# Kernel optimization log

Measured on AMD Instinct MI355X. Metric: run time of the kernel, lower is better.

## Reference

```python
import jax, jax.numpy as jnp
import numpy as np

NUM_LATENTS = 1
NUM_EMBEDDINGS = 2048
EMBEDDING_DIM = 64
DECAY = 0.99
EPS = 1e-5


def setup_inputs() -> dict:
    key = jax.random.key(0)
    k1, k2 = jax.random.split(key)
    x = jax.random.normal(k1, (65536, NUM_LATENTS * EMBEDDING_DIM), dtype=jnp.float32)
    embedding = jax.random.normal(k2, (NUM_LATENTS, NUM_EMBEDDINGS, EMBEDDING_DIM), dtype=jnp.float32)
    cluster_size = jnp.ones((NUM_LATENTS, NUM_EMBEDDINGS), dtype=jnp.float32)
    return {"input": x, "embedding": embedding, "cluster_size": cluster_size}


def reference(input, embedding, cluster_size):
    L, K, D = embedding.shape
    flat = input.reshape(-1, L, D)  # (N, L, D)
    # Squared euclidean distances (N, L, K), expanded form of (x - e)^2 sum over D
    x_sq = jnp.sum(flat * flat, axis=-1, keepdims=True)           # (N, L, 1)
    e_sq = jnp.sum(embedding * embedding, axis=-1)[None]          # (1, L, K)
    cross = jnp.einsum('nld,lkd->nlk', flat, embedding)           # (N, L, K)
    distances = x_sq - 2.0 * cross + e_sq
    encoding_indices = jnp.argmin(distances, axis=-1)             # (N, L)
    # decode: gather codebook vectors
    quantized = embedding[jnp.arange(L)[None, :], encoding_indices]  # (N, L, D)
    encodings = jax.nn.one_hot(encoding_indices, K, dtype=input.dtype)  # (N, L, K)
    # --- EMA update (training branch, non-simple, laplace smoothing) ---
    onehot_sum = jnp.sum(encodings, axis=0)                       # (L, K)
    dw = jnp.einsum('nlk,nld->lkd', encodings, flat)              # (L, K, D)
    new_cluster_size = DECAY * cluster_size + (1.0 - DECAY) * onehot_sum
    n = jnp.sum(new_cluster_size, axis=-1, keepdims=True)
    cs = (new_cluster_size + EPS) / (n + K * EPS) * n
    new_embedding = DECAY * embedding + (1.0 - DECAY) * (dw / cs[..., None])
    # --- losses / outputs ---
    q = quantized.reshape(input.shape)
    commitment_loss = jnp.mean((q - input) ** 2)
    quantized_st = input + jax.lax.stop_gradient(q - input)
    avg_probs = jnp.mean(encodings, axis=0)                       # (L, K)
    perplexity = jnp.exp(-jnp.sum(avg_probs * jnp.log(avg_probs + 1e-10) / L))
    return (quantized_st, encodings, commitment_loss, perplexity, new_embedding, new_cluster_size)
```

## Files before the change

### kernel.cpp

```cpp
#include <hip/hip_runtime.h>
#include <math.h>

#define NROWS 65536
#define KEMB  2048
#define DIM   64
#define DECAYF 0.99f
#define OMDF   0.01f
#define EPSF   1e-5f

#define WS_DW    0
#define WS_CNT   131072
#define WS_LOSS  133120
#define WS_ESQ   133632
#define WS_SCALE 135680
#define WS_IDX   137728
#define WS_SORT  203264
#define WS_START 268800
#define WS_CUR   270852

#define OUT_Q    0
#define OUT_ENC  4194304
#define OUT_LOSS 138412032
#define OUT_PERP 138412033
#define OUT_NE   138412034
#define OUT_NCS  138543106

typedef float f32x4 __attribute__((ext_vector_type(4)));

__global__ __launch_bounds__(256) void k0_prep(const float* __restrict__ x,
                                               const float* __restrict__ E,
                                               float* __restrict__ ws,
                                               float* __restrict__ out) {
    int g = blockIdx.x * 256 + threadIdx.x;
    if (g == 0) ws[WS_LOSS] = 0.f;
    if (g < 32768) {
        float4 z = make_float4(0.f, 0.f, 0.f, 0.f);
        ((float4*)(ws + WS_DW))[g] = z;
    }
    if (g < KEMB) {
        ((unsigned int*)ws)[WS_CNT + g] = 0u;
        const float4* e4 = (const float4*)(E + (size_t)g * DIM);
        float s0 = 0.f, s1 = 0.f, s2 = 0.f, s3 = 0.f;
#pragma unroll
        for (int j = 0; j < 16; j++) {
            float4 v = e4[j];
            s0 = fmaf(v.x, v.x, s0); s1 = fmaf(v.y, v.y, s1);
            s2 = fmaf(v.z, v.z, s2); s3 = fmaf(v.w, v.w, s3);
        }
        ws[WS_ESQ + g] = (s0 + s1) + (s2 + s3);
    }
    {
        const float4* x4 = (const float4*)(x + (size_t)g * DIM);
        float s0 = 0.f, s1 = 0.f, s2 = 0.f, s3 = 0.f;
#pragma unroll
        for (int j = 0; j < 16; j++) {
            float4 v = x4[j];
            s0 = fmaf(v.x, v.x, s0); s1 = fmaf(v.y, v.y, s1);
            s2 = fmaf(v.z, v.z, s2); s3 = fmaf(v.w, v.w, s3);
        }
        out[OUT_NE + g] = (s0 + s1) + (s2 + s3);
    }
}

__global__ __launch_bounds__(256, 2) void k1_main(const float* __restrict__ x,
                                                  const float* __restrict__ E,
                                                  float* __restrict__ ws,
                                                  float* __restrict__ out) {
    __shared__ float sxT[64 * 128];
    __shared__ float seT[64 * 128];

    const int t = threadIdx.x;
    const int b = blockIdx.x;
    const int tx = t & 15;
    const int ty = t >> 4;

    float xsq[8];
    {
        const float2* xs2 = (const float2*)(out + OUT_NE + (size_t)b * 128 + ty * 8);
#pragma unroll
        for (int j = 0; j < 4; j++) {
            float2 v = xs2[j];
            xsq[2 * j] = v.x; xsq[2 * j + 1] = v.y;
        }
    }

    const int kl = t & 127;
    const int dchi = t >> 7;
    {
        const float4* x4 = (const float4*)x;
#pragma unroll
        for (int i = 0; i < 8; i++) {
            int dc = dchi + 2 * i;
            float4 v = x4[((size_t)b * 128 + kl) * 16 + dc];
            sxT[(4 * dc + 0) * 128 + kl] = v.x;
            sxT[(4 * dc + 1) * 128 + kl] = v.y;
            sxT[(4 * dc + 2) * 128 + kl] = v.z;
            sxT[(4 * dc + 3) * 128 + kl] = v.w;
        }
    }

    const int c = kl >> 2;
    const int fo = (((c & 1) << 4) + (c >> 1)) * 4 + (kl & 3);
    const float4* e4 = (const float4*)E;

    float4 pv[8];
#pragma unroll
    for (int i = 0; i < 8; i++)
        pv[i] = e4[((size_t)kl) * 16 + (dchi + 2 * i)];

    float best[8];
    int bidx[8];
#pragma unroll
    for (int rr = 0; rr < 8; rr++) { best[rr] = 3.4e38f; bidx[rr] = 0; }

    f32x4* __restrict__ encz = (f32x4*)(out + OUT_ENC);
    const int g = b * 256 + t;

    for (int pass = 0; pass < 16; pass++) {
        __syncthreads();
        {
#pragma unroll
            for (int i = 0; i < 8; i++) {
                int dc = dchi + 2 * i;
                seT[(4 * dc + 0) * 128 + fo] = pv[i].x;
                seT[(4 * dc + 1) * 128 + fo] = pv[i].y;
                seT[(4 * dc + 2) * 128 + fo] = pv[i].z;
                seT[(4 * dc + 3) * 128 + fo] = pv[i].w;
            }
        }
        __syncthreads();

        if (pass < 15) {
#pragma unroll
            for (int i = 0; i < 8; i++)
                pv[i] = e4[((size_t)(pass + 1) * 128 + kl) * 16 + (dchi + 2 * i)];
        }

        {
            f32x4 z = (f32x4)(0.f);
#pragma unroll
            for (int j = 0; j < 16; j++)
                __builtin_nontemporal_store(z, encz + (size_t)(pass * 16 + j) * 131072 + g);
        }

        float acc[8][8];
#pragma unroll
        for (int rr = 0; rr < 8; rr++)
#pragma unroll
            for (int cc = 0; cc < 8; cc++) acc[rr][cc] = 0.f;

        const float* xb  = sxT + ty * 8;
        const float* ebA = seT + tx * 4;
        const float* ebB = seT + 64 + tx * 4;
#pragma unroll 2
        for (int d = 0; d < 64; d++) {
            f32x4 a0 = *(const f32x4*)(xb + d * 128);
            f32x4 a1 = *(const f32x4*)(xb + d * 128 + 4);
            f32x4 b0 = *(const f32x4*)(ebA + d * 128);
            f32x4 b1 = *(const f32x4*)(ebB + d * 128);
#pragma unroll
            for (int rr = 0; rr < 4; rr++) {
#pragma unroll
                for (int cc = 0; cc < 4; cc++) {
                    acc[rr][cc]         = fmaf(a0[rr], b0[cc], acc[rr][cc]);
                    acc[rr][cc + 4]     = fmaf(a0[rr], b1[cc], acc[rr][cc + 4]);
                    acc[rr + 4][cc]     = fmaf(a1[rr], b0[cc], acc[rr + 4][cc]);
                    acc[rr + 4][cc + 4] = fmaf(a1[rr], b1[cc], acc[rr + 4][cc + 4]);
                }
            }
        }

        const float4* esq4 = (const float4*)(ws + WS_ESQ + pass * 128 + tx * 8);
        float4 eq0 = esq4[0], eq1 = esq4[1];
        float eq[8] = {eq0.x, eq0.y, eq0.z, eq0.w, eq1.x, eq1.y, eq1.z, eq1.w};
        const int kb = pass * 128 + tx * 8;
#pragma unroll
        for (int rr = 0; rr < 8; rr++)
#pragma unroll
            for (int cc = 0; cc < 8; cc++) {
                float dist = fmaf(-2.f, acc[rr][cc], xsq[rr]) + eq[cc];
                if (dist < best[rr]) { best[rr] = dist; bidx[rr] = kb + cc; }
            }
    }

    __syncthreads();
    int* sIdx = (int*)seT;
#pragma unroll
    for (int rr = 0; rr < 8; rr++) {
        float bd = best[rr]; int bi = bidx[rr];
#pragma unroll
        for (int m = 1; m < 16; m <<= 1) {
            float od = __shfl_xor(bd, m, 64);
            int   oi = __shfl_xor(bi, m, 64);
            if (od < bd || (od == bd && oi < bi)) { bd = od; bi = oi; }
        }
        if (tx == 0) sIdx[ty * 8 + rr] = bi;
    }
    __syncthreads();

    if (t < 128) {
        const int row = b * 128 + t;
        const int bi = sIdx[t];
        ((int*)ws)[WS_IDX + row] = bi;
        atomicAdd(((unsigned int*)ws) + WS_CNT + bi, 1u);
        const float4* ebb = (const float4*)(E + (size_t)bi * DIM);
        const float4* xr4 = (const float4*)(x + (size_t)row * DIM);
        float4* qo = (float4*)(out + OUT_Q + (size_t)row * DIM);
        float l0 = 0.f, l1 = 0.f, l2 = 0.f, l3 = 0.f;
#pragma unroll
        for (int j = 0; j < 16; j++) {
            float4 ev = ebb[j];
            float4 xv = xr4[j];
            qo[j] = ev;
            float d0 = ev.x - xv.x, d1 = ev.y - xv.y;
            float d2 = ev.z - xv.z, d3 = ev.w - xv.w;
            l0 = fmaf(d0, d0, l0); l1 = fmaf(d1, d1, l1);
            l2 = fmaf(d2, d2, l2); l3 = fmaf(d3, d3, l3);
        }
        float lsum = (l0 + l1) + (l2 + l3);
#pragma unroll
        for (int o = 32; o; o >>= 1) lsum += __shfl_down(lsum, o, 64);
        if ((t & 63) == 0) unsafeAtomicAdd(ws + WS_LOSS, lsum);
    }
}

__global__ __launch_bounds__(256) void k2bs(const float* __restrict__ cs_in,
                                            float* __restrict__ ws,
                                            float* __restrict__ out) {
    __shared__ unsigned int sscan[256];
    __shared__ float sred[8];
    __shared__ float s_n;
    const int t = threadIdx.x;
    const unsigned int* cnt = ((const unsigned int*)ws) + WS_CNT;

    unsigned int c[8];
    unsigned int tot = 0;
#pragma unroll
    for (int j = 0; j < 8; j++) { c[j] = cnt[t * 8 + j]; tot += c[j]; }
    sscan[t] = tot;
    __syncthreads();
    for (int off = 1; off < 256; off <<= 1) {
        unsigned int v = (t >= off) ? sscan[t - off] : 0u;
        __syncthreads();
        sscan[t] += v;
        __syncthreads();
    }
    unsigned int run = sscan[t] - tot;
    unsigned int* starts = ((unsigned int*)ws) + WS_START;
    unsigned int* cur = ((unsigned int*)ws) + WS_CUR;
#pragma unroll
    for (int j = 0; j < 8; j++) {
        starts[t * 8 + j] = run;
        cur[t * 8 + j] = run;
        run += c[j];
    }
    if (t == 255) starts[KEMB] = run;

    float* ncs_out = out + OUT_NCS;
    float ln = 0.f, lent = 0.f;
    float ncs_v[8];
#pragma unroll
    for (int j = 0; j < 8; j++) {
        int k = t * 8 + j;
        float cf = (float)c[j];
        float ncs = DECAYF * cs_in[k] + OMDF * cf;
        ncs_out[k] = ncs;
        ncs_v[j] = ncs;
        ln += ncs;
        float p = cf * (1.0f / 65536.0f);
        lent = fmaf(p, logf(p + 1e-10f), lent);
    }
#pragma unroll
    for (int o = 32; o; o >>= 1) {
        ln += __shfl_down(ln, o, 64);
        lent += __shfl_down(lent, o, 64);
    }
    if ((t & 63) == 0) { sred[t >> 6] = ln; sred[4 + (t >> 6)] = lent; }
    __syncthreads();
    if (t == 0) {
        float n = (sred[0] + sred[1]) + (sred[2] + sred[3]);
        float ent = (sred[4] + sred[5]) + (sred[6] + sred[7]);
        s_n = n;
        out[OUT_LOSS] = ws[WS_LOSS] * (1.0f / 4194304.0f);
        out[OUT_PERP] = expf(-ent);
    }
    __syncthreads();
    float n = s_n;
    float denom = n + (float)KEMB * EPSF;
#pragma unroll
    for (int j = 0; j < 8; j++) {
        int k = t * 8 + j;
        float cs = (ncs_v[j] + EPSF) / denom * n;
        ws[WS_SCALE + k] = OMDF / cs;
    }
}

__global__ __launch_bounds__(256) void k2c_scatter(const int* __restrict__ idxp,
                                                   float* __restrict__ ws,
                                                   float* __restrict__ out) {
    const int g = blockIdx.x * 256 + threadIdx.x;
    int4 v = ((const int4*)idxp)[g];
    unsigned int* cur = ((unsigned int*)ws) + WS_CUR;
    int* sorted = ((int*)ws) + WS_SORT;
    float* __restrict__ enc = out + OUT_ENC;
    const int row = 4 * g;
    unsigned int p0 = atomicAdd(&cur[v.x], 1u);
    unsigned int p1 = atomicAdd(&cur[v.y], 1u);
    unsigned int p2 = atomicAdd(&cur[v.z], 1u);
    unsigned int p3 = atomicAdd(&cur[v.w], 1u);
    sorted[p0] = row + 0;
    sorted[p1] = row + 1;
    sorted[p2] = row + 2;
    sorted[p3] = row + 3;
    enc[(size_t)(row + 0) * KEMB + v.x] = 1.0f;
    enc[(size_t)(row + 1) * KEMB + v.y] = 1.0f;
    enc[(size_t)(row + 2) * KEMB + v.z] = 1.0f;
    enc[(size_t)(row + 3) * KEMB + v.w] = 1.0f;
}

__global__ __launch_bounds__(256) void k2d_dw(const float* __restrict__ x,
                                              const int* __restrict__ idxp,
                                              float* __restrict__ ws) {
    const int t = threadIdx.x;
    const int lane = t & 63;
    const int w = blockIdx.x * 4 + (t >> 6);
    const int base = w * 64;
    const int* sorted = ((const int*)ws) + WS_SORT;

    int rid = sorted[base + lane];
    int code_l = idxp[rid];

    float acc = 0.f;
    int cur = __shfl(code_l, 0, 64);
#pragma unroll 8
    for (int i = 0; i < 64; i++) {
        int row = __shfl(rid, i, 64);
        int code = __shfl(code_l, i, 64);
        if (code != cur) {
            unsafeAtomicAdd(ws + WS_DW + (size_t)cur * DIM + lane, acc);
            acc = 0.f;
            cur = code;
        }
        acc += x[(size_t)row * DIM + lane];
    }
    unsafeAtomicAdd(ws + WS_DW + (size_t)cur * DIM + lane, acc);
}

__global__ __launch_bounds__(256) void k4_embed(const float* __restrict__ E,
                                                const float* __restrict__ ws,
                                                float* __restrict__ out) {
    int gq = blockIdx.x * 256 + threadIdx.x;
    const float4* E4 = (const float4*)E;
    const float4* dw4 = (const float4*)(ws + WS_DW);
    float2* o2 = (float2*)(out + OUT_NE);
    int k = gq >> 4;
    float sc = ws[WS_SCALE + k];
    float4 e = E4[gq];
    float4 d = dw4[gq];
    float2 r0, r1;
    r0.x = fmaf(d.x, sc, DECAYF * e.x);
    r0.y = fmaf(d.y, sc, DECAYF * e.y);
    r1.x = fmaf(d.z, sc, DECAYF * e.z);
    r1.y = fmaf(d.w, sc, DECAYF * e.w);
    o2[2 * gq + 0] = r0;
    o2[2 * gq + 1] = r1;
}

extern "C" void kernel_launch(void* const* d_in, const int* in_sizes, int n_in,
                              void* d_out, int out_size, void* d_ws, size_t ws_size,
                              hipStream_t stream) {
    const float* x = (const float*)d_in[0];
    const float* E = (const float*)d_in[1];
    const float* cs = (const float*)d_in[2];
    float* out = (float*)d_out;
    float* ws = (float*)d_ws;
    const int* idxp = ((const int*)ws) + WS_IDX;

    hipLaunchKernelGGL(k0_prep, dim3(256), dim3(256), 0, stream, x, E, ws, out);
    hipLaunchKernelGGL(k1_main, dim3(512), dim3(256), 0, stream, x, E, ws, out);
    hipLaunchKernelGGL(k2bs, dim3(1), dim3(256), 0, stream, cs, ws, out);
    hipLaunchKernelGGL(k2c_scatter, dim3(64), dim3(256), 0, stream, idxp, ws, out);
    hipLaunchKernelGGL(k2d_dw, dim3(256), dim3(256), 0, stream, x, idxp, ws);
    hipLaunchKernelGGL(k4_embed, dim3(128), dim3(256), 0, stream, E, ws, out);
}
```

Measured before the change: 294.4 us.

## Widen codebook tile to 256 codes and fuse row norms and one-hot writes

The distance kernel now processes 256 codebook entries per pass, using an 8x16 register tile per thread and two 32-wide depth halves staged through shared memory. This raises FMA work per shared-memory load and halves the number of passes. Row squared norms are now computed in k1_main while x is loaded into shared memory, so k0_prep no longer reads x. The one-hot 1.0 is written in k1_main right after that block zeroes its own encoding rows, which removes the scatter write from k2c_scatter. The cost is much higher register pressure from 128 accumulators per thread, which could cause spills or lower occupancy.

```diff
diff --git a/kernel.cpp b/kernel.cpp
--- a/kernel.cpp
+++ b/kernel.cpp
@@ -27,16 +27,11 @@
 
 typedef float f32x4 __attribute__((ext_vector_type(4)));
 
-__global__ __launch_bounds__(256) void k0_prep(const float* __restrict__ x,
-                                               const float* __restrict__ E,
-                                               float* __restrict__ ws,
-                                               float* __restrict__ out) {
+__global__ __launch_bounds__(256) void k0_prep(const float* __restrict__ E,
+                                               float* __restrict__ ws) {
     int g = blockIdx.x * 256 + threadIdx.x;
     if (g == 0) ws[WS_LOSS] = 0.f;
-    if (g < 32768) {
-        float4 z = make_float4(0.f, 0.f, 0.f, 0.f);
-        ((float4*)(ws + WS_DW))[g] = z;
-    }
+    ((float4*)(ws + WS_DW))[g] = make_float4(0.f, 0.f, 0.f, 0.f);
     if (g < KEMB) {
         ((unsigned int*)ws)[WS_CNT + g] = 0u;
         const float4* e4 = (const float4*)(E + (size_t)g * DIM);
@@ -48,17 +43,6 @@
             s2 = fmaf(v.z, v.z, s2); s3 = fmaf(v.w, v.w, s3);
         }
         ws[WS_ESQ + g] = (s0 + s1) + (s2 + s3);
-    }
-    {
-        const float4* x4 = (const float4*)(x + (size_t)g * DIM);
-        float s0 = 0.f, s1 = 0.f, s2 = 0.f, s3 = 0.f;
-#pragma unroll
-        for (int j = 0; j < 16; j++) {
-            float4 v = x4[j];
-            s0 = fmaf(v.x, v.x, s0); s1 = fmaf(v.y, v.y, s1);
-            s2 = fmaf(v.z, v.z, s2); s3 = fmaf(v.w, v.w, s3);
-        }
-        out[OUT_NE + g] = (s0 + s1) + (s2 + s3);
     }
 }
 
@@ -67,46 +51,47 @@
                                                   float* __restrict__ ws,
                                                   float* __restrict__ out) {
     __shared__ float sxT[64 * 128];
-    __shared__ float seT[64 * 128];
+    __shared__ float seT[32 * 256];
+    __shared__ float sxq[256];
 
     const int t = threadIdx.x;
     const int b = blockIdx.x;
     const int tx = t & 15;
     const int ty = t >> 4;
 
+    {
+        const int rl = t & 127;
+        const int dhi2 = t >> 7;
+        const float4* x4 = (const float4*)x;
+        float s0 = 0.f, s1 = 0.f, s2 = 0.f, s3 = 0.f;
+#pragma unroll
+        for (int i = 0; i < 8; i++) {
+            int dc = dhi2 + 2 * i;
+            float4 v = x4[((size_t)b * 128 + rl) * 16 + dc];
+            sxT[(4 * dc + 0) * 128 + rl] = v.x;
+            sxT[(4 * dc + 1) * 128 + rl] = v.y;
+            sxT[(4 * dc + 2) * 128 + rl] = v.z;
+            sxT[(4 * dc + 3) * 128 + rl] = v.w;
+            s0 = fmaf(v.x, v.x, s0); s1 = fmaf(v.y, v.y, s1);
+            s2 = fmaf(v.z, v.z, s2); s3 = fmaf(v.w, v.w, s3);
+        }
+        sxq[dhi2 * 128 + rl] = (s0 + s1) + (s2 + s3);
+    }
+
+    const int sbase = (((t >> 2) & 3) << 6) + ((t >> 4) << 2) + (t & 3);
+    const float4* e4 = (const float4*)E;
+
+    float4 pv[8];
+#pragma unroll
+    for (int j = 0; j < 8; j++)
+        pv[j] = e4[(size_t)t * 16 + j];
+
+    __syncthreads();
+
     float xsq[8];
-    {
-        const float2* xs2 = (const float2*)(out + OUT_NE + (size_t)b * 128 + ty * 8);
-#pragma unroll
-        for (int j = 0; j < 4; j++) {
-            float2 v = xs2[j];
-            xsq[2 * j] = v.x; xsq[2 * j + 1] = v.y;
-        }
-    }
-
-    const int kl = t & 127;
-    const int dchi = t >> 7;
-    {
-        const float4* x4 = (const float4*)x;
-#pragma unroll
-        for (int i = 0; i < 8; i++) {
-            int dc = dchi + 2 * i;
-            float4 v = x4[((size_t)b * 128 + kl) * 16 + dc];
-            sxT[(4 * dc + 0) * 128 + kl] = v.x;
-            sxT[(4 * dc + 1) * 128 + kl] = v.y;
-            sxT[(4 * dc + 2) * 128 + kl] = v.z;
-            sxT[(4 * dc + 3) * 128 + kl] = v.w;
-        }
-    }
-
-    const int c = kl >> 2;
-    const int fo = (((c & 1) << 4) + (c >> 1)) * 4 + (kl & 3);
-    const float4* e4 = (const float4*)E;
-
-    float4 pv[8];
-#pragma unroll
-    for (int i = 0; i < 8; i++)
-        pv[i] = e4[((size_t)kl) * 16 + (dchi + 2 * i)];
+#pragma unroll
+    for (int rr = 0; rr < 8; rr++)
+        xsq[rr] = sxq[ty * 8 + rr] + sxq[128 + ty * 8 + rr];
 
     float best[8];
     int bidx[8];
@@ -114,77 +99,84 @@
     for (int rr = 0; rr < 8; rr++) { best[rr] = 3.4e38f; bidx[rr] = 0; }
 
     f32x4* __restrict__ encz = (f32x4*)(out + OUT_ENC);
-    const int g = b * 256 + t;
-
-    for (int pass = 0; pass < 16; pass++) {
-        __syncthreads();
-        {
-#pragma unroll
-            for (int i = 0; i < 8; i++) {
-                int dc = dchi + 2 * i;
-                seT[(4 * dc + 0) * 128 + fo] = pv[i].x;
-                seT[(4 * dc + 1) * 128 + fo] = pv[i].y;
-                seT[(4 * dc + 2) * 128 + fo] = pv[i].z;
-                seT[(4 * dc + 3) * 128 + fo] = pv[i].w;
-            }
-        }
-        __syncthreads();
-
-        if (pass < 15) {
-#pragma unroll
-            for (int i = 0; i < 8; i++)
-                pv[i] = e4[((size_t)(pass + 1) * 128 + kl) * 16 + (dchi + 2 * i)];
-        }
-
-        {
-            f32x4 z = (f32x4)(0.f);
-#pragma unroll
-            for (int j = 0; j < 16; j++)
-                __builtin_nontemporal_store(z, encz + (size_t)(pass * 16 + j) * 131072 + g);
-        }
-
-        float acc[8][8];
+
+    for (int pass = 0; pass < 8; pass++) {
+        float acc[8][16];
 #pragma unroll
         for (int rr = 0; rr < 8; rr++)
 #pragma unroll
-            for (int cc = 0; cc < 8; cc++) acc[rr][cc] = 0.f;
-
-        const float* xb  = sxT + ty * 8;
-        const float* ebA = seT + tx * 4;
-        const float* ebB = seT + 64 + tx * 4;
-#pragma unroll 2
-        for (int d = 0; d < 64; d++) {
-            f32x4 a0 = *(const f32x4*)(xb + d * 128);
-            f32x4 a1 = *(const f32x4*)(xb + d * 128 + 4);
-            f32x4 b0 = *(const f32x4*)(ebA + d * 128);
-            f32x4 b1 = *(const f32x4*)(ebB + d * 128);
-#pragma unroll
-            for (int rr = 0; rr < 4; rr++) {
-#pragma unroll
-                for (int cc = 0; cc < 4; cc++) {
-                    acc[rr][cc]         = fmaf(a0[rr], b0[cc], acc[rr][cc]);
-                    acc[rr][cc + 4]     = fmaf(a0[rr], b1[cc], acc[rr][cc + 4]);
-                    acc[rr + 4][cc]     = fmaf(a1[rr], b0[cc], acc[rr + 4][cc]);
-                    acc[rr + 4][cc + 4] = fmaf(a1[rr], b1[cc], acc[rr + 4][cc + 4]);
+            for (int m = 0; m < 16; m++) acc[rr][m] = 0.f;
+
+        for (int dh = 0; dh < 2; dh++) {
+            if (pass + dh) __syncthreads();
+#pragma unroll
+            for (int j = 0; j < 8; j++) {
+                seT[(4 * j + 0) * 256 + sbase] = pv[j].x;
+                seT[(4 * j + 1) * 256 + sbase] = pv[j].y;
+                seT[(4 * j + 2) * 256 + sbase] = pv[j].z;
+                seT[(4 * j + 3) * 256 + sbase] = pv[j].w;
+            }
+            __syncthreads();
+
+            {
+                int h = pass * 2 + dh + 1;
+                if (h < 16) {
+#pragma unroll
+                    for (int j = 0; j < 8; j++)
+                        pv[j] = e4[((size_t)((h >> 1) * 256 + t)) * 16 + (h & 1) * 8 + j];
                 }
             }
-        }
-
-        const float4* esq4 = (const float4*)(ws + WS_ESQ + pass * 128 + tx * 8);
-        float4 eq0 = esq4[0], eq1 = esq4[1];
-        float eq[8] = {eq0.x, eq0.y, eq0.z, eq0.w, eq1.x, eq1.y, eq1.z, eq1.w};
-        const int kb = pass * 128 + tx * 8;
+
+            if (dh == 0) {
+                f32x4 z = (f32x4)(0.f);
+#pragma unroll
+                for (int j = 0; j < 32; j++)
+                    __builtin_nontemporal_store(z,
+                        encz + (size_t)b * 65536 + pass * 8192 + j * 256 + t);
+            }
+
+            const float* xbase = sxT + dh * 32 * 128 + ty * 8;
+            for (int dd = 0; dd < 32; dd++) {
+                const float* sb = seT + dd * 256;
+                f32x4 a0 = *(const f32x4*)(xbase + dd * 128);
+                f32x4 a1 = *(const f32x4*)(xbase + dd * 128 + 4);
+                f32x4 b0 = *(const f32x4*)(sb + tx * 4);
+                f32x4 b1 = *(const f32x4*)(sb + 64 + tx * 4);
+                f32x4 b2 = *(const f32x4*)(sb + 128 + tx * 4);
+                f32x4 b3 = *(const f32x4*)(sb + 192 + tx * 4);
+#pragma unroll
+                for (int rr = 0; rr < 4; rr++) {
+#pragma unroll
+                    for (int cc = 0; cc < 4; cc++) {
+                        acc[rr][cc]          = fmaf(a0[rr], b0[cc], acc[rr][cc]);
+                        acc[rr][4 + cc]      = fmaf(a0[rr], b1[cc], acc[rr][4 + cc]);
+                        acc[rr][8 + cc]      = fmaf(a0[rr], b2[cc], acc[rr][8 + cc]);
+                        acc[rr][12 + cc]     = fmaf(a0[rr], b3[cc], acc[rr][12 + cc]);
+                        acc[4 + rr][cc]      = fmaf(a1[rr], b0[cc], acc[4 + rr][cc]);
+                        acc[4 + rr][4 + cc]  = fmaf(a1[rr], b1[cc], acc[4 + rr][4 + cc]);
+                        acc[4 + rr][8 + cc]  = fmaf(a1[rr], b2[cc], acc[4 + rr][8 + cc]);
+                        acc[4 + rr][12 + cc] = fmaf(a1[rr], b3[cc], acc[4 + rr][12 + cc]);
+                    }
+                }
+            }
+        }
+
+        const float4* esq4 = (const float4*)(ws + WS_ESQ + pass * 256 + tx * 16);
+        float4 eqv0 = esq4[0], eqv1 = esq4[1], eqv2 = esq4[2], eqv3 = esq4[3];
+        float eq[16] = {eqv0.x, eqv0.y, eqv0.z, eqv0.w, eqv1.x, eqv1.y, eqv1.z, eqv1.w,
+                        eqv2.x, eqv2.y, eqv2.z, eqv2.w, eqv3.x, eqv3.y, eqv3.z, eqv3.w};
+        const int kb = pass * 256 + tx * 16;
 #pragma unroll
         for (int rr = 0; rr < 8; rr++)
 #pragma unroll
-            for (int cc = 0; cc < 8; cc++) {
-                float dist = fmaf(-2.f, acc[rr][cc], xsq[rr]) + eq[cc];
-                if (dist < best[rr]) { best[rr] = dist; bidx[rr] = kb + cc; }
-            }
-    }
-
-    __syncthreads();
-    int* sIdx = (int*)seT;
+            for (int m = 0; m < 16; m++) {
+                float dist = fmaf(-2.f, acc[rr][m], xsq[rr]) + eq[m];
+                if (dist < best[rr]) { best[rr] = dist; bidx[rr] = kb + m; }
+            }
+    }
+
+    __syncthreads();
+    int* sIdx = (int*)sxq;
 #pragma unroll
     for (int rr = 0; rr < 8; rr++) {
         float bd = best[rr]; int bi = bidx[rr];
@@ -203,6 +195,7 @@
         const int bi = sIdx[t];
         ((int*)ws)[WS_IDX + row] = bi;
         atomicAdd(((unsigned int*)ws) + WS_CNT + bi, 1u);
+        out[OUT_ENC + (size_t)row * KEMB + bi] = 1.0f;
         const float4* ebb = (const float4*)(E + (size_t)bi * DIM);
         const float4* xr4 = (const float4*)(x + (size_t)row * DIM);
         float4* qo = (float4*)(out + OUT_Q + (size_t)row * DIM);
@@ -296,13 +289,11 @@
 }
 
 __global__ __launch_bounds__(256) void k2c_scatter(const int* __restrict__ idxp,
-                                                   float* __restrict__ ws,
-                                                   float* __restrict__ out) {
+                                                   float* __restrict__ ws) {
     const int g = blockIdx.x * 256 + threadIdx.x;
     int4 v = ((const int4*)idxp)[g];
     unsigned int* cur = ((unsigned int*)ws) + WS_CUR;
     int* sorted = ((int*)ws) + WS_SORT;
-    float* __restrict__ enc = out + OUT_ENC;
     const int row = 4 * g;
     unsigned int p0 = atomicAdd(&cur[v.x], 1u);
     unsigned int p1 = atomicAdd(&cur[v.y], 1u);
@@ -312,10 +303,6 @@
     sorted[p1] = row + 1;
     sorted[p2] = row + 2;
     sorted[p3] = row + 3;
-    enc[(size_t)(row + 0) * KEMB + v.x] = 1.0f;
-    enc[(size_t)(row + 1) * KEMB + v.y] = 1.0f;
-    enc[(size_t)(row + 2) * KEMB + v.z] = 1.0f;
-    enc[(size_t)(row + 3) * KEMB + v.w] = 1.0f;
 }
 
 __global__ __launch_bounds__(256) void k2d_dw(const float* __restrict__ x,
@@ -376,10 +363,10 @@
     float* ws = (float*)d_ws;
     const int* idxp = ((const int*)ws) + WS_IDX;
 
-    hipLaunchKernelGGL(k0_prep, dim3(256), dim3(256), 0, stream, x, E, ws, out);
+    hipLaunchKernelGGL(k0_prep, dim3(128), dim3(256), 0, stream, E, ws);
     hipLaunchKernelGGL(k1_main, dim3(512), dim3(256), 0, stream, x, E, ws, out);
     hipLaunchKernelGGL(k2bs, dim3(1), dim3(256), 0, stream, cs, ws, out);
-    hipLaunchKernelGGL(k2c_scatter, dim3(64), dim3(256), 0, stream, idxp, ws, out);
+    hipLaunchKernelGGL(k2c_scatter, dim3(64), dim3(256), 0, stream, idxp, ws);
     hipLaunchKernelGGL(k2d_dw, dim3(256), dim3(256), 0, stream, x, idxp, ws);
     hipLaunchKernelGGL(k4_embed, dim3(128), dim3(256), 0, stream, E, ws, out);
 }
```

New measurement: 295.9 us. No clear change (+0.5%).
